# Kernel tuning notes

Hardware: AMD Instinct MI355X
Metric: run time of the kernel (lower is better)

The kernel has to match this reference:

```python
import jax, jax.numpy as jnp
import numpy as np

NUM_EMBEDDINGS = 1024
EMBEDDING_DIM = 256
E_LOSS_WEIGHT = 0.25
MU = 0.01
EPSILON = 1e-05
N_TOKENS = 65536


def setup_inputs() -> dict:
    key = jax.random.key(0)
    k1, k2, k3 = jax.random.split(key, 3)
    return {
        "inputs": jax.random.normal(k1, (N_TOKENS, EMBEDDING_DIM), dtype=jnp.float32),
        "embedding_weight": jax.random.normal(k2, (NUM_EMBEDDINGS, EMBEDDING_DIM), dtype=jnp.float32),
        "ema_w": jax.random.normal(k3, (NUM_EMBEDDINGS, EMBEDDING_DIM), dtype=jnp.float32),
        "ema_cluster_size": jnp.zeros((NUM_EMBEDDINGS,), dtype=jnp.float32),
    }


def reference(inputs, embedding_weight, ema_w, ema_cluster_size):
    N, D = inputs.shape
    K = embedding_weight.shape[0]

    # Squared L2 distances: [N, K]
    distances = (
        jnp.sum(inputs ** 2, axis=1, keepdims=True)
        + jnp.sum(embedding_weight ** 2, axis=1)
        - 2.0 * (inputs @ embedding_weight.T)
    )
    idx = jnp.argmin(distances, axis=1)              # [N]

    # Gather codebook entries (replaces one-hot @ weight)
    quantized_raw = embedding_weight[idx]            # [N, D]

    # Commitment loss (quantized detached)
    e_latent_loss = jnp.mean((jax.lax.stop_gradient(quantized_raw) - inputs) ** 2)
    loss = E_LOSS_WEIGHT * e_latent_loss

    # Per-code counts and scatter-sum of inputs (replaces one-hot matmuls)
    counts = jax.ops.segment_sum(jnp.ones((N,), inputs.dtype), idx, num_segments=K)  # [K]
    dw = jax.ops.segment_sum(inputs, idx, num_segments=K)                             # [K, D]

    # EMA updates (training branch)
    new_cluster = ema_cluster_size * (1.0 - MU) + MU * counts
    n = jnp.sum(new_cluster)
    new_cluster = (new_cluster + EPSILON) / (n + K * EPSILON) * n
    new_ema_w = ema_w * (1.0 - MU) + MU * dw
    new_embedding = new_ema_w / new_cluster[:, None]

    # Straight-through estimator
    quantized = inputs + jax.lax.stop_gradient(quantized_raw - inputs)

    avg_probs = counts / N
    perplexity = jnp.exp(-jnp.sum(avg_probs * jnp.log(avg_probs + 1e-10)))

    encoding_indices = idx.reshape(N, 1)
    return quantized, loss, encoding_indices, perplexity, new_cluster, new_ema_w, new_embedding
```

## Files before the change

kernel.cpp:

```cpp
#include <hip/hip_runtime.h>

typedef _Float16 half8 __attribute__((ext_vector_type(8)));
typedef _Float16 half4 __attribute__((ext_vector_type(4)));
typedef float f32x4 __attribute__((ext_vector_type(4)));

#define N_TOK 65536
#define DIM   256
#define KCODE 1024
#define MU_C  0.01f
#define EPS_C 1e-5f

#define O_Q    0
#define O_LOSS 16777216
#define O_IDX  16777217
#define O_PERP 16842753
#define O_NC   16842754
#define O_NEW  16843778
#define O_EMB  17105922

#define W_IDX   0
#define W_CNT   65536
#define W_CUR   66560
#define W_OFF   67584
#define W_CNTF  68608
#define W_NFLAG 69632
#define W_ELAT  69633
#define W_FLAG  69696
#define W_ORDER 135232
#define W_DW    200768
#define W_WSQ   462912
#define W_WH    463936
#define W_XSQF  595008
#define W_ELATA 660544
#define W_PACK  676928

__device__ __forceinline__ int imin(int a, int b) { return a < b ? a : b; }
__device__ __forceinline__ int imax(int a, int b) { return a > b ? a : b; }

__global__ void convert_wsq(const float* __restrict__ W, _Float16* __restrict__ Wh,
                            float* __restrict__ wsq) {
    int gid = blockIdx.x * 256 + threadIdx.x;
    int row = gid >> 6, lane = gid & 63;
    float4 v = *(const float4*)(W + (size_t)row * 256 + lane * 4);
    half4 h;
    h[0] = (_Float16)v.x; h[1] = (_Float16)v.y; h[2] = (_Float16)v.z; h[3] = (_Float16)v.w;
    *(half4*)(Wh + (size_t)row * 256 + lane * 4) = h;
    float s = v.x * v.x + v.y * v.y + v.z * v.z + v.w * v.w;
#pragma unroll
    for (int off = 1; off < 64; off <<= 1) s += __shfl_xor(s, off);
    if (lane == 0) wsq[row] = s;
}

__global__ __launch_bounds__(256, 2) void argmin_mfma(
    const float* __restrict__ X, const _Float16* __restrict__ Wh,
    const float* __restrict__ wsq, int* __restrict__ idx_out,
    unsigned* __restrict__ nflag, int* __restrict__ flaglist)
{
    __shared__ _Float16 Bs[2][64 * 256];

    const int tid  = threadIdx.x;
    const int lane = tid & 63;
    const int w    = tid >> 6;
    const int l15  = lane & 15;
    const int lk   = lane >> 4;
    const int t0   = blockIdx.x * 128;

    half8 a[2][8];
#pragma unroll
    for (int mf = 0; mf < 2; ++mf) {
        const float* xr = X + (size_t)(t0 + w * 32 + mf * 16 + l15) * 256 + lk * 8;
#pragma unroll
        for (int g = 0; g < 8; ++g) {
            float4 u0 = *(const float4*)(xr + g * 32);
            float4 u1 = *(const float4*)(xr + g * 32 + 4);
            half8 h;
            h[0] = (_Float16)u0.x; h[1] = (_Float16)u0.y;
            h[2] = (_Float16)u0.z; h[3] = (_Float16)u0.w;
            h[4] = (_Float16)u1.x; h[5] = (_Float16)u1.y;
            h[6] = (_Float16)u1.z; h[7] = (_Float16)u1.w;
            a[mf][g] = h;
        }
    }

    int u1a[8], u2a[8];
#pragma unroll
    for (int i = 0; i < 8; ++i) { u1a[i] = 0x7FFFFFFF; u2a[i] = 0x7FFFFFFF; }

#define STAGE(cc, bb)                                                          \
    _Pragma("unroll")                                                          \
    for (int i = 0; i < 8; ++i) {                                              \
        int loff = (w * 8 + i) * 1024;                                         \
        int off  = loff + lane * 16;                                           \
        int row  = off >> 9;                                                   \
        int slot = (off >> 4) & 31;                                            \
        const _Float16* src = Wh + (size_t)((cc) * 64 + row) * 256             \
                                 + ((slot ^ (row & 7)) << 3);                  \
        __builtin_amdgcn_global_load_lds(                                      \
            (const __attribute__((address_space(1))) void*)src,                \
            (__attribute__((address_space(3))) void*)((char*)Bs[bb] + loff),   \
            16, 0, 0);                                                         \
    }

    STAGE(0, 0);
    __syncthreads();

    for (int c = 0; c < 16; ++c) {
        const int cur = c & 1;
        if (c < 15) { STAGE(c + 1, cur ^ 1); }

        f32x4 acc[2][4];
#pragma unroll
        for (int mf = 0; mf < 2; ++mf)
#pragma unroll
            for (int nf = 0; nf < 4; ++nf) acc[mf][nf] = (f32x4)0.0f;

#pragma unroll
        for (int ks = 0; ks < 4; ++ks) {
#pragma unroll
            for (int kk = 0; kk < 2; ++kk) {
                half8 b4[4];
#pragma unroll
                for (int nf = 0; nf < 4; ++nf) {
                    int row  = nf * 16 + l15;
                    int slot = ks * 8 + kk * 4 + lk;
                    b4[nf] = *(const half8*)((const char*)Bs[cur]
                              + row * 512 + ((slot ^ (row & 7)) << 4));
                }
#pragma unroll
                for (int nf = 0; nf < 4; ++nf) {
                    acc[0][nf] = __builtin_amdgcn_mfma_f32_16x16x32_f16(
                        a[0][ks * 2 + kk], b4[nf], acc[0][nf], 0, 0, 0);
                    acc[1][nf] = __builtin_amdgcn_mfma_f32_16x16x32_f16(
                        a[1][ks * 2 + kk], b4[nf], acc[1][nf], 0, 0, 0);
                }
            }
        }
#pragma unroll
        for (int nf = 0; nf < 4; ++nf) {
            int   code = c * 64 + nf * 16 + l15;
            float tc   = fmaf(0.5f, wsq[code], 512.0f);
#pragma unroll
            for (int mf = 0; mf < 2; ++mf)
#pragma unroll
                for (int r = 0; r < 4; ++r) {
                    float sv = tc - acc[mf][nf][r];
                    int u = (__float_as_int(sv) & 0xFFFFFC00) | code;
                    int s8 = mf * 4 + r;
                    u2a[s8] = imin(u2a[s8], imax(u1a[s8], u));
                    u1a[s8] = imin(u1a[s8], u);
                }
        }
        __syncthreads();
    }
#undef STAGE

#pragma unroll
    for (int s8 = 0; s8 < 8; ++s8) {
#pragma unroll
        for (int off = 1; off < 16; off <<= 1) {
            int b1 = __shfl_xor(u1a[s8], off);
            int b2 = __shfl_xor(u2a[s8], off);
            int n2 = imin(imin(u2a[s8], b2), imax(u1a[s8], b1));
            u1a[s8] = imin(u1a[s8], b1);
            u2a[s8] = n2;
        }
    }
    if (l15 == 0) {
#pragma unroll
        for (int s8 = 0; s8 < 8; ++s8) {
            int mf = s8 >> 2, r = s8 & 3;
            int row = t0 + w * 32 + mf * 16 + lk * 4 + r;
            idx_out[row] = u1a[s8] & 1023;
            float s1 = __int_as_float(u1a[s8] & 0xFFFFFC00);
            float s2 = __int_as_float(u2a[s8] & 0xFFFFFC00);
            if (s2 - s1 < 0.125f) {
                unsigned p = atomicAdd(nflag, 1u);
                flaglist[p] = row;
            }
        }
    }
}

__global__ void cleanup_xsq(const float* __restrict__ X,
                            const unsigned* __restrict__ nflagp,
                            const int* __restrict__ flaglist,
                            float* __restrict__ xsqf) {
    int n = (int)nflagp[0];
    int wid  = (blockIdx.x * 256 + threadIdx.x) >> 6;
    int lane = threadIdx.x & 63;
    for (int i = wid; i < n; i += 1024) {
        const float* row = X + (size_t)flaglist[i] * 256;
        float4 v = *(const float4*)(row + lane * 4);
        float s = v.x * v.x + v.y * v.y + v.z * v.z + v.w * v.w;
#pragma unroll
        for (int off = 1; off < 64; off <<= 1) s += __shfl_xor(s, off);
        if (lane == 0) xsqf[i] = s;
    }
}

#define BM 128
#define BK 16

__global__ __launch_bounds__(256) void cleanup_gemm(
    const float* __restrict__ X, const float* __restrict__ W,
    const float* __restrict__ wsq, const unsigned* __restrict__ nflagp,
    const int* __restrict__ flaglist, const float* __restrict__ xsqf,
    unsigned long long* __restrict__ pack)
{
    __shared__ float xs [BK][BM];
    __shared__ float wps[BK][128];
    __shared__ float wsq_s[128];

    const int n = (int)nflagp[0];
    const int tid  = threadIdx.x;
    const int tx   = tid & 15;
    const int ty   = tid >> 4;
    const int trow = tid >> 1;
    const int khalf = (tid & 1) * 8;
    const int c0   = (blockIdx.x & 7) * 128;

    for (int tile = blockIdx.x >> 3; tile * BM < n; tile += 64) {
        const int t0 = tile * BM;
        const int gtok = flaglist[imin(t0 + trow, n - 1)];

        float xsq_r[8];
#pragma unroll
        for (int i = 0; i < 8; ++i) xsq_r[i] = xsqf[imin(t0 + ty * 8 + i, n - 1)];

        float minv[8]; int mini[8];
#pragma unroll
        for (int i = 0; i < 8; ++i) { minv[i] = 3.402823466e+38f; mini[i] = 0; }

        float acc[8][8];
#pragma unroll
        for (int i = 0; i < 8; ++i)
#pragma unroll
            for (int j = 0; j < 8; ++j) acc[i][j] = 0.0f;

        for (int ks = 0; ks < DIM / BK; ++ks) {
            const int kb = ks * BK;
            __syncthreads();
            {
                const float* xr = X + (size_t)gtok * DIM + kb + khalf;
                float4 v0 = *(const float4*)xr;
                float4 v1 = *(const float4*)(xr + 4);
                xs[khalf + 0][trow] = v0.x; xs[khalf + 1][trow] = v0.y;
                xs[khalf + 2][trow] = v0.z; xs[khalf + 3][trow] = v0.w;
                xs[khalf + 4][trow] = v1.x; xs[khalf + 5][trow] = v1.y;
                xs[khalf + 6][trow] = v1.z; xs[khalf + 7][trow] = v1.w;
                const float* wr = W + (size_t)(c0 + trow) * DIM + kb + khalf;
                float4 u0 = *(const float4*)wr;
                float4 u1 = *(const float4*)(wr + 4);
                wps[khalf + 0][trow] = u0.x; wps[khalf + 1][trow] = u0.y;
                wps[khalf + 2][trow] = u0.z; wps[khalf + 3][trow] = u0.w;
                wps[khalf + 4][trow] = u1.x; wps[khalf + 5][trow] = u1.y;
                wps[khalf + 6][trow] = u1.z; wps[khalf + 7][trow] = u1.w;
                if (ks == 0 && tid < 128) wsq_s[tid] = wsq[c0 + tid];
            }
            __syncthreads();
#pragma unroll
            for (int kl = 0; kl < BK; ++kl) {
                float4 a0 = *(const float4*)&xs [kl][ty * 8];
                float4 a1 = *(const float4*)&xs [kl][ty * 8 + 4];
                float4 b0 = *(const float4*)&wps[kl][tx * 8];
                float4 b1 = *(const float4*)&wps[kl][tx * 8 + 4];
                float a[8] = {a0.x, a0.y, a0.z, a0.w, a1.x, a1.y, a1.z, a1.w};
                float b[8] = {b0.x, b0.y, b0.z, b0.w, b1.x, b1.y, b1.z, b1.w};
#pragma unroll
                for (int i = 0; i < 8; ++i)
#pragma unroll
                    for (int j = 0; j < 8; ++j)
                        acc[i][j] = fmaf(a[i], b[j], acc[i][j]);
            }
        }
#pragma unroll
        for (int i = 0; i < 8; ++i) {
#pragma unroll
            for (int j = 0; j < 8; ++j) {
                float t1 = xsq_r[i] + wsq_s[tx * 8 + j];
                float s  = t1 - 2.0f * acc[i][j];
                int   c  = c0 + tx * 8 + j;
                if (s < minv[i]) { minv[i] = s; mini[i] = c; }
            }
        }
#pragma unroll
        for (int i = 0; i < 8; ++i) {
#pragma unroll
            for (int off = 1; off < 16; off <<= 1) {
                float ov = __shfl_xor(minv[i], off);
                int   oi = __shfl_xor(mini[i], off);
                if (ov < minv[i] || (ov == minv[i] && oi < mini[i])) {
                    minv[i] = ov; mini[i] = oi;
                }
            }
        }
        if (tx == 0) {
#pragma unroll
            for (int i = 0; i < 8; ++i) {
                int pos = t0 + ty * 8 + i;
                if (pos < n) {
                    unsigned long long pu =
                        ((unsigned long long)(unsigned)__float_as_int(minv[i]) << 32)
                        | (unsigned)mini[i];
                    atomicMin(&pack[pos], pu);
                }
            }
        }
        __syncthreads();
    }
}

__global__ void cleanup_write(const unsigned* __restrict__ nflagp,
                              const int* __restrict__ flaglist,
                              const unsigned long long* __restrict__ pack,
                              int* __restrict__ idx_out) {
    int n = (int)nflagp[0];
    for (int i = blockIdx.x * 256 + threadIdx.x; i < n; i += 65536)
        idx_out[flaglist[i]] = (int)(pack[i] & 0xFFFFFFFFull);
}

__global__ void k_hist(const int* __restrict__ idx, unsigned* __restrict__ cnt) {
    int t = blockIdx.x * 256 + threadIdx.x;
    atomicAdd(&cnt[idx[t]], 1u);
}

__global__ __launch_bounds__(1024) void k_scan(const unsigned* __restrict__ cnt,
                                               unsigned* __restrict__ offs,
                                               float* __restrict__ cntf) {
    __shared__ unsigned s[1024];
    int k = threadIdx.x;
    unsigned v = cnt[k];
    s[k] = v; cntf[k] = (float)v;
    __syncthreads();
    for (int d = 1; d < 1024; d <<= 1) {
        unsigned add = (k >= d) ? s[k - d] : 0u;
        __syncthreads();
        s[k] += add;
        __syncthreads();
    }
    offs[k] = s[k] - v;
}

__global__ void k_scatter(const int* __restrict__ idx, const unsigned* __restrict__ offs,
                          unsigned* __restrict__ cursor, int* __restrict__ order) {
    int t = blockIdx.x * 256 + threadIdx.x;
    int c = idx[t];
    unsigned p = atomicAdd(&cursor[c], 1u);
    order[offs[c] + p] = t;
}

__global__ __launch_bounds__(256) void k_dw(const float* __restrict__ X,
                                            const int* __restrict__ order,
                                            const int* __restrict__ idx,
                                            float* __restrict__ dw)
{
    int gw   = (blockIdx.x * 256 + threadIdx.x) >> 6;
    int lane = threadIdx.x & 63;
    int p0 = gw * 16;
    float4 acc = make_float4(0.f, 0.f, 0.f, 0.f);
    int cur = -1;
#pragma unroll 4
    for (int i = 0; i < 16; ++i) {
        int t = order[p0 + i];
        int c = idx[t];
        float4 x4 = *(const float4*)(X + (size_t)t * 256 + lane * 4);
        if (c != cur) {
            if (cur >= 0) {
                float* dwp = dw + (size_t)cur * 256 + lane * 4;
                atomicAdd(dwp + 0, acc.x); atomicAdd(dwp + 1, acc.y);
                atomicAdd(dwp + 2, acc.z); atomicAdd(dwp + 3, acc.w);
            }
            cur = c; acc = x4;
        } else {
            acc.x += x4.x; acc.y += x4.y; acc.z += x4.z; acc.w += x4.w;
        }
    }
    if (cur >= 0) {
        float* dwp = dw + (size_t)cur * 256 + lane * 4;
        atomicAdd(dwp + 0, acc.x); atomicAdd(dwp + 1, acc.y);
        atomicAdd(dwp + 2, acc.z); atomicAdd(dwp + 3, acc.w);
    }
}

__global__ __launch_bounds__(256) void epilogue_token(
    const float* __restrict__ X, const float* __restrict__ W,
    const int* __restrict__ idx, float* __restrict__ out,
    float* __restrict__ elat_arr)
{
    int gid = blockIdx.x * 256 + threadIdx.x;
    int t = gid >> 6, q = gid & 63;
    int code = idx[t];
    float4 x4 = ((const float4*)X)[gid];
    float4 w4 = ((const float4*)W)[(size_t)code * 64 + q];
    ((float4*)(out + O_Q))[gid] = w4;
    float dx0 = w4.x - x4.x, dx1 = w4.y - x4.y, dx2 = w4.z - x4.z, dx3 = w4.w - x4.w;
    float e = dx0 * dx0 + dx1 * dx1 + dx2 * dx2 + dx3 * dx3;
    if (q == 0) out[O_IDX + t] = (float)code;
#pragma unroll
    for (int off = 1; off < 64; off <<= 1) e += __shfl_xor(e, off);
    __shared__ float se[4];
    int lane = threadIdx.x & 63, wid = threadIdx.x >> 6;
    if (lane == 0) se[wid] = e;
    __syncthreads();
    if (threadIdx.x == 0) elat_arr[blockIdx.x] = se[0] + se[1] + se[2] + se[3];
}

__global__ __launch_bounds__(1024) void finalize_small(
    const float* __restrict__ ecs, const float* __restrict__ counts,
    const float* __restrict__ elat_arr, float* __restrict__ out)
{
    int k = threadIdx.x;
    float cnt = counts[k];
    float nc = ecs[k] * (1.0f - MU_C) + MU_C * cnt;
    float p = cnt * (1.0f / 65536.0f);
    float h = p * logf(p + 1e-10f);
    float el = 0.f;
#pragma unroll
    for (int i = 0; i < 16; ++i) el += elat_arr[k + i * 1024];
    float rn = nc, rh = h, re = el;
#pragma unroll
    for (int off = 1; off < 64; off <<= 1) {
        rn += __shfl_xor(rn, off);
        rh += __shfl_xor(rh, off);
        re += __shfl_xor(re, off);
    }
    __shared__ float sn[16], sh[16], sef[16];
    int wid = k >> 6, lane = k & 63;
    if (lane == 0) { sn[wid] = rn; sh[wid] = rh; sef[wid] = re; }
    __syncthreads();
    float n = 0.0f, H = 0.0f, E = 0.0f;
#pragma unroll
    for (int i = 0; i < 16; ++i) { n += sn[i]; H += sh[i]; E += sef[i]; }
    out[O_NC + k] = (nc + EPS_C) / (n + 1024.0f * EPS_C) * n;
    if (k == 0) {
        out[O_LOSS] = 0.25f * (E * (1.0f / 16777216.0f));
        out[O_PERP] = expf(-H);
    }
}

__global__ void finalize_embed(const float* __restrict__ ema_w,
                               const float* __restrict__ dw, float* __restrict__ out)
{
    int gid = blockIdx.x * blockDim.x + threadIdx.x;
    int k = gid >> 8;
    float ew = ema_w[gid] * (1.0f - MU_C) + MU_C * dw[gid];
    out[O_NEW + gid] = ew;
    out[O_EMB + gid] = ew / out[O_NC + k];
}

extern "C" void kernel_launch(void* const* d_in, const int* in_sizes, int n_in,
                              void* d_out, int out_size, void* d_ws, size_t ws_size,
                              hipStream_t stream) {
    const float* X     = (const float*)d_in[0];
    const float* W     = (const float*)d_in[1];
    const float* ema_w = (const float*)d_in[2];
    const float* ecs   = (const float*)d_in[3];
    float*    out    = (float*)d_out;
    unsigned* wsu    = (unsigned*)d_ws;
    float*    wsf    = (float*)d_ws;
    int*      idx    = (int*)d_ws + W_IDX;
    unsigned* cnt    = wsu + W_CNT;
    unsigned* cursor = wsu + W_CUR;
    unsigned* offs   = wsu + W_OFF;
    float*    cntf   = wsf + W_CNTF;
    unsigned* nflag  = wsu + W_NFLAG;
    int*      flags  = (int*)d_ws + W_FLAG;
    int*      order  = (int*)d_ws + W_ORDER;
    float*    dw     = wsf + W_DW;
    float*    wsq    = wsf + W_WSQ;
    _Float16* Wh     = (_Float16*)(wsu + W_WH);
    float*    xsqf   = wsf + W_XSQF;
    float*    elatA  = wsf + W_ELATA;
    unsigned long long* pack = (unsigned long long*)(wsu + W_PACK);

    hipMemsetAsync(wsu + W_CNT, 0, 4098 * sizeof(unsigned), stream);
    hipMemsetAsync(wsf + W_DW,  0, 262144 * sizeof(float),  stream);
    hipMemsetAsync(pack, 0xFF, 65536 * sizeof(unsigned long long), stream);
    hipLaunchKernelGGL(convert_wsq,    dim3(256),   dim3(256),  0, stream, W, Wh, wsq);
    hipLaunchKernelGGL(argmin_mfma,    dim3(512),   dim3(256),  0, stream, X, Wh, wsq, idx, nflag, flags);
    hipLaunchKernelGGL(cleanup_xsq,    dim3(256),   dim3(256),  0, stream, X, nflag, flags, xsqf);
    hipLaunchKernelGGL(cleanup_gemm,   dim3(512),   dim3(256),  0, stream, X, W, wsq, nflag, flags, xsqf, pack);
    hipLaunchKernelGGL(cleanup_write,  dim3(256),   dim3(256),  0, stream, nflag, flags, pack, idx);
    hipLaunchKernelGGL(k_hist,         dim3(256),   dim3(256),  0, stream, idx, cnt);
    hipLaunchKernelGGL(k_scan,         dim3(1),     dim3(1024), 0, stream, cnt, offs, cntf);
    hipLaunchKernelGGL(k_scatter,      dim3(256),   dim3(256),  0, stream, idx, offs, cursor, order);
    hipLaunchKernelGGL(k_dw,           dim3(1024),  dim3(256),  0, stream, X, order, idx, dw);
    hipLaunchKernelGGL(epilogue_token, dim3(16384), dim3(256),  0, stream, X, W, idx, out, elatA);
    hipLaunchKernelGGL(finalize_small, dim3(1),     dim3(1024), 0, stream, ecs, cntf, elatA, out);
    hipLaunchKernelGGL(finalize_embed, dim3(1024),  dim3(256),  0, stream, ema_w, dw, out);
}
```

Before: 256.4 us.

## Shrink argmin and cleanup tiles, fuse histogram into epilogue, warp-scan offsets

```diff
diff --git a/kernel.cpp b/kernel.cpp
--- a/kernel.cpp
+++ b/kernel.cpp
@@ -51,24 +51,23 @@
     if (lane == 0) wsq[row] = s;
 }
 
-__global__ __launch_bounds__(256, 2) void argmin_mfma(
+__global__ __launch_bounds__(256, 4) void argmin_mfma(
     const float* __restrict__ X, const _Float16* __restrict__ Wh,
     const float* __restrict__ wsq, int* __restrict__ idx_out,
     unsigned* __restrict__ nflag, int* __restrict__ flaglist)
 {
-    __shared__ _Float16 Bs[2][64 * 256];
+    __shared__ _Float16 Bs[2][32 * 256];
 
     const int tid  = threadIdx.x;
     const int lane = tid & 63;
     const int w    = tid >> 6;
     const int l15  = lane & 15;
     const int lk   = lane >> 4;
-    const int t0   = blockIdx.x * 128;
-
-    half8 a[2][8];
-#pragma unroll
-    for (int mf = 0; mf < 2; ++mf) {
-        const float* xr = X + (size_t)(t0 + w * 32 + mf * 16 + l15) * 256 + lk * 8;
+    const int t0   = blockIdx.x * 64;
+
+    half8 a[8];
+    {
+        const float* xr = X + (size_t)(t0 + w * 16 + l15) * 256 + lk * 8;
 #pragma unroll
         for (int g = 0; g < 8; ++g) {
             float4 u0 = *(const float4*)(xr + g * 32);
@@ -78,22 +77,22 @@
             h[2] = (_Float16)u0.z; h[3] = (_Float16)u0.w;
             h[4] = (_Float16)u1.x; h[5] = (_Float16)u1.y;
             h[6] = (_Float16)u1.z; h[7] = (_Float16)u1.w;
-            a[mf][g] = h;
-        }
-    }
-
-    int u1a[8], u2a[8];
-#pragma unroll
-    for (int i = 0; i < 8; ++i) { u1a[i] = 0x7FFFFFFF; u2a[i] = 0x7FFFFFFF; }
+            a[g] = h;
+        }
+    }
+
+    int u1a[4], u2a[4];
+#pragma unroll
+    for (int i = 0; i < 4; ++i) { u1a[i] = 0x7FFFFFFF; u2a[i] = 0x7FFFFFFF; }
 
 #define STAGE(cc, bb)                                                          \
     _Pragma("unroll")                                                          \
-    for (int i = 0; i < 8; ++i) {                                              \
-        int loff = (w * 8 + i) * 1024;                                         \
+    for (int i = 0; i < 4; ++i) {                                              \
+        int loff = (w * 4 + i) * 1024;                                         \
         int off  = loff + lane * 16;                                           \
         int row  = off >> 9;                                                   \
         int slot = (off >> 4) & 31;                                            \
-        const _Float16* src = Wh + (size_t)((cc) * 64 + row) * 256             \
+        const _Float16* src = Wh + (size_t)((cc) * 32 + row) * 256             \
                                  + ((slot ^ (row & 7)) << 3);                  \
         __builtin_amdgcn_global_load_lds(                                      \
             (const __attribute__((address_space(1))) void*)src,                \
@@ -104,75 +103,64 @@
     STAGE(0, 0);
     __syncthreads();
 
-    for (int c = 0; c < 16; ++c) {
+    for (int c = 0; c < 32; ++c) {
         const int cur = c & 1;
-        if (c < 15) { STAGE(c + 1, cur ^ 1); }
-
-        f32x4 acc[2][4];
-#pragma unroll
-        for (int mf = 0; mf < 2; ++mf)
-#pragma unroll
-            for (int nf = 0; nf < 4; ++nf) acc[mf][nf] = (f32x4)0.0f;
-
+        if (c < 31) { STAGE(c + 1, cur ^ 1); }
+
+        f32x4 acc[2];
+        acc[0] = (f32x4)0.0f; acc[1] = (f32x4)0.0f;
+
+        __builtin_amdgcn_s_setprio(1);
 #pragma unroll
         for (int ks = 0; ks < 4; ++ks) {
 #pragma unroll
             for (int kk = 0; kk < 2; ++kk) {
-                half8 b4[4];
-#pragma unroll
-                for (int nf = 0; nf < 4; ++nf) {
-                    int row  = nf * 16 + l15;
-                    int slot = ks * 8 + kk * 4 + lk;
-                    b4[nf] = *(const half8*)((const char*)Bs[cur]
-                              + row * 512 + ((slot ^ (row & 7)) << 4));
-                }
-#pragma unroll
-                for (int nf = 0; nf < 4; ++nf) {
-                    acc[0][nf] = __builtin_amdgcn_mfma_f32_16x16x32_f16(
-                        a[0][ks * 2 + kk], b4[nf], acc[0][nf], 0, 0, 0);
-                    acc[1][nf] = __builtin_amdgcn_mfma_f32_16x16x32_f16(
-                        a[1][ks * 2 + kk], b4[nf], acc[1][nf], 0, 0, 0);
-                }
-            }
-        }
-#pragma unroll
-        for (int nf = 0; nf < 4; ++nf) {
-            int   code = c * 64 + nf * 16 + l15;
+                int slot = ks * 8 + kk * 4 + lk;
+                int sw   = (slot ^ (l15 & 7)) << 4;
+                half8 b0 = *(const half8*)((const char*)Bs[cur] + l15 * 512 + sw);
+                half8 b1 = *(const half8*)((const char*)Bs[cur] + (16 + l15) * 512 + sw);
+                acc[0] = __builtin_amdgcn_mfma_f32_16x16x32_f16(
+                    a[ks * 2 + kk], b0, acc[0], 0, 0, 0);
+                acc[1] = __builtin_amdgcn_mfma_f32_16x16x32_f16(
+                    a[ks * 2 + kk], b1, acc[1], 0, 0, 0);
+            }
+        }
+        __builtin_amdgcn_s_setprio(0);
+
+#pragma unroll
+        for (int nf = 0; nf < 2; ++nf) {
+            int   code = c * 32 + nf * 16 + l15;
             float tc   = fmaf(0.5f, wsq[code], 512.0f);
 #pragma unroll
-            for (int mf = 0; mf < 2; ++mf)
-#pragma unroll
-                for (int r = 0; r < 4; ++r) {
-                    float sv = tc - acc[mf][nf][r];
-                    int u = (__float_as_int(sv) & 0xFFFFFC00) | code;
-                    int s8 = mf * 4 + r;
-                    u2a[s8] = imin(u2a[s8], imax(u1a[s8], u));
-                    u1a[s8] = imin(u1a[s8], u);
-                }
+            for (int r = 0; r < 4; ++r) {
+                float sv = tc - acc[nf][r];
+                int u = (__float_as_int(sv) & 0xFFFFFC00) | code;
+                u2a[r] = imin(u2a[r], imax(u1a[r], u));
+                u1a[r] = imin(u1a[r], u);
+            }
         }
         __syncthreads();
     }
 #undef STAGE
 
 #pragma unroll
-    for (int s8 = 0; s8 < 8; ++s8) {
+    for (int r = 0; r < 4; ++r) {
 #pragma unroll
         for (int off = 1; off < 16; off <<= 1) {
-            int b1 = __shfl_xor(u1a[s8], off);
-            int b2 = __shfl_xor(u2a[s8], off);
-            int n2 = imin(imin(u2a[s8], b2), imax(u1a[s8], b1));
-            u1a[s8] = imin(u1a[s8], b1);
-            u2a[s8] = n2;
+            int b1 = __shfl_xor(u1a[r], off);
+            int b2 = __shfl_xor(u2a[r], off);
+            int n2 = imin(imin(u2a[r], b2), imax(u1a[r], b1));
+            u1a[r] = imin(u1a[r], b1);
+            u2a[r] = n2;
         }
     }
     if (l15 == 0) {
 #pragma unroll
-        for (int s8 = 0; s8 < 8; ++s8) {
-            int mf = s8 >> 2, r = s8 & 3;
-            int row = t0 + w * 32 + mf * 16 + lk * 4 + r;
-            idx_out[row] = u1a[s8] & 1023;
-            float s1 = __int_as_float(u1a[s8] & 0xFFFFFC00);
-            float s2 = __int_as_float(u2a[s8] & 0xFFFFFC00);
+        for (int r = 0; r < 4; ++r) {
+            int row = t0 + w * 16 + lk * 4 + r;
+            idx_out[row] = u1a[r] & 1023;
+            float s1 = __int_as_float(u1a[r] & 0xFFFFFC00);
+            float s2 = __int_as_float(u2a[r] & 0xFFFFFC00);
             if (s2 - s1 < 0.125f) {
                 unsigned p = atomicAdd(nflag, 1u);
                 flaglist[p] = row;
@@ -198,93 +186,91 @@
     }
 }
 
-#define BM 128
-#define BK 16
-
-__global__ __launch_bounds__(256) void cleanup_gemm(
+__global__ __launch_bounds__(256, 2) void cleanup_gemm(
     const float* __restrict__ X, const float* __restrict__ W,
     const float* __restrict__ wsq, const unsigned* __restrict__ nflagp,
     const int* __restrict__ flaglist, const float* __restrict__ xsqf,
     unsigned long long* __restrict__ pack)
 {
-    __shared__ float xs [BK][BM];
-    __shared__ float wps[BK][128];
+    __shared__ float xs [16][64];
+    __shared__ float wps[16][128];
     __shared__ float wsq_s[128];
 
     const int n = (int)nflagp[0];
-    const int tid  = threadIdx.x;
-    const int tx   = tid & 15;
-    const int ty   = tid >> 4;
-    const int trow = tid >> 1;
-    const int khalf = (tid & 1) * 8;
-    const int c0   = (blockIdx.x & 7) * 128;
-
-    for (int tile = blockIdx.x >> 3; tile * BM < n; tile += 64) {
-        const int t0 = tile * BM;
-        const int gtok = flaglist[imin(t0 + trow, n - 1)];
-
-        float xsq_r[8];
-#pragma unroll
-        for (int i = 0; i < 8; ++i) xsq_r[i] = xsqf[imin(t0 + ty * 8 + i, n - 1)];
-
-        float minv[8]; int mini[8];
-#pragma unroll
-        for (int i = 0; i < 8; ++i) { minv[i] = 3.402823466e+38f; mini[i] = 0; }
-
-        float acc[8][8];
-#pragma unroll
-        for (int i = 0; i < 8; ++i)
+    const int tid = threadIdx.x;
+    const int tx  = tid & 15;
+    const int ty  = tid >> 4;
+    const int c0    = (blockIdx.x & 7) * 128;
+    const int tslot = blockIdx.x >> 3;
+    const int srow_x = tid & 63,  sq_x = tid >> 6;
+    const int srow_w = tid & 127, sh_w = tid >> 7;
+
+    if (tid < 128) wsq_s[tid] = wsq[c0 + tid];
+
+    for (int tile = tslot; tile * 64 < n; tile += 256) {
+        const int t0 = tile * 64;
+        const int gtok = flaglist[imin(t0 + srow_x, n - 1)];
+        const float* xrow = X + (size_t)gtok * DIM;
+        const float* wrow = W + (size_t)(c0 + srow_w) * DIM + sh_w * 8;
+
+        float xsq_r[4];
+#pragma unroll
+        for (int i = 0; i < 4; ++i) xsq_r[i] = xsqf[imin(t0 + ty * 4 + i, n - 1)];
+
+        float minv[4]; int mini[4];
+#pragma unroll
+        for (int i = 0; i < 4; ++i) { minv[i] = 3.402823466e+38f; mini[i] = 0; }
+
+        float acc[4][8];
+#pragma unroll
+        for (int i = 0; i < 4; ++i)
 #pragma unroll
             for (int j = 0; j < 8; ++j) acc[i][j] = 0.0f;
 
-        for (int ks = 0; ks < DIM / BK; ++ks) {
-            const int kb = ks * BK;
+        float4 xa = *(const float4*)(xrow + sq_x * 4);
+        float4 wa = *(const float4*)(wrow);
+        float4 wb = *(const float4*)(wrow + 4);
+
+        for (int ks = 0; ks < 16; ++ks) {
             __syncthreads();
-            {
-                const float* xr = X + (size_t)gtok * DIM + kb + khalf;
-                float4 v0 = *(const float4*)xr;
-                float4 v1 = *(const float4*)(xr + 4);
-                xs[khalf + 0][trow] = v0.x; xs[khalf + 1][trow] = v0.y;
-                xs[khalf + 2][trow] = v0.z; xs[khalf + 3][trow] = v0.w;
-                xs[khalf + 4][trow] = v1.x; xs[khalf + 5][trow] = v1.y;
-                xs[khalf + 6][trow] = v1.z; xs[khalf + 7][trow] = v1.w;
-                const float* wr = W + (size_t)(c0 + trow) * DIM + kb + khalf;
-                float4 u0 = *(const float4*)wr;
-                float4 u1 = *(const float4*)(wr + 4);
-                wps[khalf + 0][trow] = u0.x; wps[khalf + 1][trow] = u0.y;
-                wps[khalf + 2][trow] = u0.z; wps[khalf + 3][trow] = u0.w;
-                wps[khalf + 4][trow] = u1.x; wps[khalf + 5][trow] = u1.y;
-                wps[khalf + 6][trow] = u1.z; wps[khalf + 7][trow] = u1.w;
-                if (ks == 0 && tid < 128) wsq_s[tid] = wsq[c0 + tid];
-            }
+            xs[sq_x * 4 + 0][srow_x] = xa.x; xs[sq_x * 4 + 1][srow_x] = xa.y;
+            xs[sq_x * 4 + 2][srow_x] = xa.z; xs[sq_x * 4 + 3][srow_x] = xa.w;
+            wps[sh_w * 8 + 0][srow_w] = wa.x; wps[sh_w * 8 + 1][srow_w] = wa.y;
+            wps[sh_w * 8 + 2][srow_w] = wa.z; wps[sh_w * 8 + 3][srow_w] = wa.w;
+            wps[sh_w * 8 + 4][srow_w] = wb.x; wps[sh_w * 8 + 5][srow_w] = wb.y;
+            wps[sh_w * 8 + 6][srow_w] = wb.z; wps[sh_w * 8 + 7][srow_w] = wb.w;
             __syncthreads();
-#pragma unroll
-            for (int kl = 0; kl < BK; ++kl) {
-                float4 a0 = *(const float4*)&xs [kl][ty * 8];
-                float4 a1 = *(const float4*)&xs [kl][ty * 8 + 4];
+            if (ks < 15) {
+                xa = *(const float4*)(xrow + (ks + 1) * 16 + sq_x * 4);
+                wa = *(const float4*)(wrow + (ks + 1) * 16);
+                wb = *(const float4*)(wrow + (ks + 1) * 16 + 4);
+            }
+#pragma unroll
+            for (int kl = 0; kl < 16; ++kl) {
+                float4 av = *(const float4*)&xs [kl][ty * 4];
                 float4 b0 = *(const float4*)&wps[kl][tx * 8];
                 float4 b1 = *(const float4*)&wps[kl][tx * 8 + 4];
-                float a[8] = {a0.x, a0.y, a0.z, a0.w, a1.x, a1.y, a1.z, a1.w};
-                float b[8] = {b0.x, b0.y, b0.z, b0.w, b1.x, b1.y, b1.z, b1.w};
-#pragma unroll
-                for (int i = 0; i < 8; ++i)
+                float aa[4] = {av.x, av.y, av.z, av.w};
+                float bb[8] = {b0.x, b0.y, b0.z, b0.w, b1.x, b1.y, b1.z, b1.w};
+#pragma unroll
+                for (int i = 0; i < 4; ++i)
 #pragma unroll
                     for (int j = 0; j < 8; ++j)
-                        acc[i][j] = fmaf(a[i], b[j], acc[i][j]);
-            }
-        }
-#pragma unroll
-        for (int i = 0; i < 8; ++i) {
+                        acc[i][j] = fmaf(aa[i], bb[j], acc[i][j]);
+            }
+        }
+#pragma unroll
+        for (int i = 0; i < 4; ++i) {
 #pragma unroll
             for (int j = 0; j < 8; ++j) {
                 float t1 = xsq_r[i] + wsq_s[tx * 8 + j];
                 float s  = t1 - 2.0f * acc[i][j];
-                int   c  = c0 + tx * 8 + j;
-                if (s < minv[i]) { minv[i] = s; mini[i] = c; }
-            }
-        }
-#pragma unroll
-        for (int i = 0; i < 8; ++i) {
+                int   cc = c0 + tx * 8 + j;
+                if (s < minv[i]) { minv[i] = s; mini[i] = cc; }
+            }
+        }
+#pragma unroll
+        for (int i = 0; i < 4; ++i) {
 #pragma unroll
             for (int off = 1; off < 16; off <<= 1) {
                 float ov = __shfl_xor(minv[i], off);
@@ -296,8 +282,8 @@
         }
         if (tx == 0) {
 #pragma unroll
-            for (int i = 0; i < 8; ++i) {
-                int pos = t0 + ty * 8 + i;
+            for (int i = 0; i < 4; ++i) {
+                int pos = t0 + ty * 4 + i;
                 if (pos < n) {
                     unsigned long long pu =
                         ((unsigned long long)(unsigned)__float_as_int(minv[i]) << 32)
@@ -319,26 +305,57 @@
         idx_out[flaglist[i]] = (int)(pack[i] & 0xFFFFFFFFull);
 }
 
-__global__ void k_hist(const int* __restrict__ idx, unsigned* __restrict__ cnt) {
-    int t = blockIdx.x * 256 + threadIdx.x;
-    atomicAdd(&cnt[idx[t]], 1u);
-}
-
-__global__ __launch_bounds__(1024) void k_scan(const unsigned* __restrict__ cnt,
-                                               unsigned* __restrict__ offs,
-                                               float* __restrict__ cntf) {
-    __shared__ unsigned s[1024];
-    int k = threadIdx.x;
-    unsigned v = cnt[k];
-    s[k] = v; cntf[k] = (float)v;
+__global__ __launch_bounds__(256) void epilogue_token(
+    const float* __restrict__ X, const float* __restrict__ W,
+    const int* __restrict__ idx, float* __restrict__ out,
+    float* __restrict__ elat_arr, unsigned* __restrict__ cnt)
+{
+    int gid = blockIdx.x * 256 + threadIdx.x;
+    int t = gid >> 6, q = gid & 63;
+    int code = idx[t];
+    float4 x4 = ((const float4*)X)[gid];
+    float4 w4 = ((const float4*)W)[(size_t)code * 64 + q];
+    ((float4*)(out + O_Q))[gid] = w4;
+    float dx0 = w4.x - x4.x, dx1 = w4.y - x4.y, dx2 = w4.z - x4.z, dx3 = w4.w - x4.w;
+    float e = dx0 * dx0 + dx1 * dx1 + dx2 * dx2 + dx3 * dx3;
+    if (q == 0) {
+        out[O_IDX + t] = (float)code;
+        atomicAdd(&cnt[code], 1u);
+    }
+#pragma unroll
+    for (int off = 1; off < 64; off <<= 1) e += __shfl_xor(e, off);
+    __shared__ float se[4];
+    int lane = threadIdx.x & 63, wid = threadIdx.x >> 6;
+    if (lane == 0) se[wid] = e;
     __syncthreads();
-    for (int d = 1; d < 1024; d <<= 1) {
-        unsigned add = (k >= d) ? s[k - d] : 0u;
-        __syncthreads();
-        s[k] += add;
-        __syncthreads();
-    }
-    offs[k] = s[k] - v;
+    if (threadIdx.x == 0) elat_arr[blockIdx.x] = se[0] + se[1] + se[2] + se[3];
+}
+
+__global__ __launch_bounds__(256) void k_scan(const unsigned* __restrict__ cnt,
+                                              unsigned* __restrict__ offs,
+                                              float* __restrict__ cntf) {
+    int t = threadIdx.x, lane = t & 63, wid = t >> 6;
+    uint4 v = ((const uint4*)cnt)[t];
+    cntf[4 * t + 0] = (float)v.x; cntf[4 * t + 1] = (float)v.y;
+    cntf[4 * t + 2] = (float)v.z; cntf[4 * t + 3] = (float)v.w;
+    unsigned s = v.x + v.y + v.z + v.w;
+    unsigned ps = s;
+#pragma unroll
+    for (int off = 1; off < 64; off <<= 1) {
+        unsigned o = __shfl_up(ps, off);
+        if (lane >= off) ps += o;
+    }
+    __shared__ unsigned wsum[4];
+    if (lane == 63) wsum[wid] = ps;
+    __syncthreads();
+    unsigned base = 0;
+#pragma unroll
+    for (int i = 0; i < 4; ++i) if (i < wid) base += wsum[i];
+    unsigned excl = base + ps - s;
+    offs[4 * t + 0] = excl;
+    offs[4 * t + 1] = excl + v.x;
+    offs[4 * t + 2] = excl + v.x + v.y;
+    offs[4 * t + 3] = excl + v.x + v.y + v.z;
 }
 
 __global__ void k_scatter(const int* __restrict__ idx, const unsigned* __restrict__ offs,
@@ -380,29 +397,6 @@
         atomicAdd(dwp + 0, acc.x); atomicAdd(dwp + 1, acc.y);
         atomicAdd(dwp + 2, acc.z); atomicAdd(dwp + 3, acc.w);
     }
-}
-
-__global__ __launch_bounds__(256) void epilogue_token(
-    const float* __restrict__ X, const float* __restrict__ W,
-    const int* __restrict__ idx, float* __restrict__ out,
-    float* __restrict__ elat_arr)
-{
-    int gid = blockIdx.x * 256 + threadIdx.x;
-    int t = gid >> 6, q = gid & 63;
-    int code = idx[t];
-    float4 x4 = ((const float4*)X)[gid];
-    float4 w4 = ((const float4*)W)[(size_t)code * 64 + q];
-    ((float4*)(out + O_Q))[gid] = w4;
-    float dx0 = w4.x - x4.x, dx1 = w4.y - x4.y, dx2 = w4.z - x4.z, dx3 = w4.w - x4.w;
-    float e = dx0 * dx0 + dx1 * dx1 + dx2 * dx2 + dx3 * dx3;
-    if (q == 0) out[O_IDX + t] = (float)code;
-#pragma unroll
-    for (int off = 1; off < 64; off <<= 1) e += __shfl_xor(e, off);
-    __shared__ float se[4];
-    int lane = threadIdx.x & 63, wid = threadIdx.x >> 6;
-    if (lane == 0) se[wid] = e;
-    __syncthreads();
-    if (threadIdx.x == 0) elat_arr[blockIdx.x] = se[0] + se[1] + se[2] + se[3];
 }
 
 __global__ __launch_bounds__(1024) void finalize_small(
@@ -477,15 +471,14 @@
     hipMemsetAsync(wsf + W_DW,  0, 262144 * sizeof(float),  stream);
     hipMemsetAsync(pack, 0xFF, 65536 * sizeof(unsigned long long), stream);
     hipLaunchKernelGGL(convert_wsq,    dim3(256),   dim3(256),  0, stream, W, Wh, wsq);
-    hipLaunchKernelGGL(argmin_mfma,    dim3(512),   dim3(256),  0, stream, X, Wh, wsq, idx, nflag, flags);
+    hipLaunchKernelGGL(argmin_mfma,    dim3(1024),  dim3(256),  0, stream, X, Wh, wsq, idx, nflag, flags);
     hipLaunchKernelGGL(cleanup_xsq,    dim3(256),   dim3(256),  0, stream, X, nflag, flags, xsqf);
-    hipLaunchKernelGGL(cleanup_gemm,   dim3(512),   dim3(256),  0, stream, X, W, wsq, nflag, flags, xsqf, pack);
+    hipLaunchKernelGGL(cleanup_gemm,   dim3(2048),  dim3(256),  0, stream, X, W, wsq, nflag, flags, xsqf, pack);
     hipLaunchKernelGGL(cleanup_write,  dim3(256),   dim3(256),  0, stream, nflag, flags, pack, idx);
-    hipLaunchKernelGGL(k_hist,         dim3(256),   dim3(256),  0, stream, idx, cnt);
-    hipLaunchKernelGGL(k_scan,         dim3(1),     dim3(1024), 0, stream, cnt, offs, cntf);
+    hipLaunchKernelGGL(epilogue_token, dim3(16384), dim3(256),  0, stream, X, W, idx, out, elatA, cnt);
+    hipLaunchKernelGGL(k_scan,         dim3(1),     dim3(256),  0, stream, cnt, offs, cntf);
     hipLaunchKernelGGL(k_scatter,      dim3(256),   dim3(256),  0, stream, idx, offs, cursor, order);
     hipLaunchKernelGGL(k_dw,           dim3(1024),  dim3(256),  0, stream, X, order, idx, dw);
-    hipLaunchKernelGGL(epilogue_token, dim3(16384), dim3(256),  0, stream, X, W, idx, out, elatA);
     hipLaunchKernelGGL(finalize_small, dim3(1),     dim3(1024), 0, stream, ecs, cntf, elatA, out);
     hipLaunchKernelGGL(finalize_embed, dim3(1024),  dim3(256),  0, stream, ema_w, dw, out);
 }
```

Measured after the change: 233.7 us. 1.1x faster.
